# Optimization experiments

Measured on AMD Instinct MI355X. Metric: run time of the kernel, lower is better.

The kernel has to match this reference:

```python
import jax, jax.numpy as jnp
import numpy as np
import math

# irreps: (multiplicity, l). Parities omitted (they only label output irreps, not the math).
X_IRREPS = [(64, 0), (64, 1), (64, 2)]   # dim 64*(1+3+5) = 576
Y_IRREPS = [(1, 0), (1, 1), (1, 2)]      # dim 9 (spherical-harmonic-like features)
N = 32768


def _cg(j1, m1, j2, m2, j3, m3):
    """Condon-Shortley Clebsch-Gordan <j1 m1 j2 m2 | j3 m3> (Racah formula)."""
    if m1 + m2 != m3:
        return 0.0
    f = math.factorial
    pre = (2 * j3 + 1) * f(j3 + j1 - j2) * f(j3 - j1 + j2) * f(j1 + j2 - j3) / f(j1 + j2 + j3 + 1)
    pre *= f(j3 + m3) * f(j3 - m3) * f(j1 - m1) * f(j1 + m1) * f(j2 - m2) * f(j2 + m2)
    s = 0.0
    for k in range(0, j1 + j2 - j3 + 1):
        d = [j1 + j2 - j3 - k, j1 - m1 - k, j2 + m2 - k, j3 - j2 + m1 + k, j3 - j1 - m2 + k]
        if min(d) < 0:
            continue
        s += (-1) ** k / (f(k) * f(d[0]) * f(d[1]) * f(d[2]) * f(d[3]) * f(d[4]))
    return math.sqrt(pre) * s


def _w3j_complex(l1, l2, l3):
    """Wigner 3j in the complex spherical basis, index m+l."""
    C = np.zeros((2 * l1 + 1, 2 * l2 + 1, 2 * l3 + 1), dtype=np.complex128)
    for m1 in range(-l1, l1 + 1):
        for m2 in range(-l2, l2 + 1):
            m3 = -(m1 + m2)
            if abs(m3) > l3:
                continue
            C[m1 + l1, m2 + l2, m3 + l3] = ((-1) ** (l1 - l2 - m3)) / math.sqrt(2 * l3 + 1) * _cg(l1, m1, l2, m2, l3, -m3)
    return C


def _Q(l):
    """Complex->real spherical harmonics change of basis (unitary)."""
    q = np.zeros((2 * l + 1, 2 * l + 1), dtype=np.complex128)
    q[l, l] = 1.0
    s2 = 1.0 / math.sqrt(2.0)
    for m in range(1, l + 1):
        q[l + m, l - m] = s2
        q[l + m, l + m] = ((-1) ** m) * s2
        q[l - m, l - m] = 1j * s2
        q[l - m, l + m] = -1j * ((-1) ** m) * s2
    return q


def _w3j_real(l1, l2, l3):
    """Real-basis Wigner 3j: invariant under real irreps; unit Frobenius norm 1/sqrt(2l3+1) preserved."""
    T = np.einsum('ia,jb,kc,abc->ijk', _Q(l1), _Q(l2), _Q(l3), _w3j_complex(l1, l2, l3))
    re, im = np.real(T), np.imag(T)
    W = re if np.abs(re).sum() >= np.abs(im).sum() else im
    return np.ascontiguousarray(W.astype(np.float32))


W3J = {}
for _mu, _l1 in X_IRREPS:
    for _mv, _l2 in Y_IRREPS:
        for _l3 in range(abs(_l1 - _l2), _l1 + _l2 + 1):
            if (_l1, _l2, _l3) not in W3J:
                W3J[(_l1, _l2, _l3)] = jnp.asarray(_w3j_real(_l1, _l2, _l3))


def _splits(irreps):
    out, off = [], 0
    for mul, l in irreps:
        d = mul * (2 * l + 1)
        out.append((mul, l, off, off + d))
        off += d
    return out


def setup_inputs() -> dict:
    key = jax.random.key(0)
    kx, ky = jax.random.split(key)
    x = jax.random.normal(kx, (N, 576), dtype=jnp.float32)
    y = jax.random.normal(ky, (N, 9), dtype=jnp.float32)
    return {"x": x, "y": y}


def reference(x, y):
    """Full e3nn-style tensor product with 'component' normalization (alpha = sqrt(2*l3+1)).
    Output chunks are concatenated in (l1, l2, l3) iteration order."""
    chunks = []
    for mu, l1, a1, b1 in _splits(X_IRREPS):
        xc = x[:, a1:b1].reshape(-1, mu, 2 * l1 + 1)
        for mv, l2, a2, b2 in _splits(Y_IRREPS):
            yc = y[:, a2:b2].reshape(-1, mv, 2 * l2 + 1)
            for l3 in range(abs(l1 - l2), l1 + l2 + 1):
                w = W3J[(l1, l2, l3)]
                alpha = np.float32(math.sqrt(2 * l3 + 1))
                z = jnp.einsum('nui,nvj,ijk->nuvk', xc, yc, w) * alpha
                chunks.append(z.reshape(z.shape[0], mu * mv * (2 * l3 + 1)))
    return jnp.concatenate(chunks, axis=-1)
```

## Files before the change

kernel.cpp:

```cpp
#include <hip/hip_runtime.h>


#define NP 19

constexpr int P_L1[NP]  = {0,0,0, 1,1,1,1,1,1,1, 2,2,2,2,2,2,2,2,2};
constexpr int P_L2[NP]  = {0,1,2, 0,1,1,1,2,2,2, 0,1,1,1,2,2,2,2,2};
constexpr int P_L3[NP]  = {0,1,2, 1,0,1,2,1,2,3, 2,1,2,3,0,1,2,3,4};
constexpr int P_WOFF[NP] = {0,1,10,35,44,53,80,125,170,245,350,375,420,495,600,625,700,825,1000};
constexpr int P_ZOFF[NP] = {0,64,256,576,768,832,1024,1344,1536,1856,2304,2624,2816,3136,3584,3648,3840,4160,4608};
constexpr int WTOT = 1225;
constexpr int XD = 576, YD = 9, ZD = 5184;


__device__ inline double dfact(int n){ double r=1.0; for(int i=2;i<=n;++i) r*=(double)i; return r; }

__device__ double cgc(int j1,int m1,int j2,int m2,int j3,int m3){
  if (m1+m2 != m3) return 0.0;
  double pre = (double)(2*j3+1) * dfact(j3+j1-j2)*dfact(j3-j1+j2)*dfact(j1+j2-j3)/dfact(j1+j2+j3+1);
  pre *= dfact(j3+m3)*dfact(j3-m3)*dfact(j1-m1)*dfact(j1+m1)*dfact(j2-m2)*dfact(j2+m2);
  double s = 0.0;
  for (int k=0;k<=j1+j2-j3;++k){
    int d0=j1+j2-j3-k, d1=j1-m1-k, d2=j2+m2-k, d3=j3-j2+m1+k, d4=j3-j1-m2+k;
    if (d0<0||d1<0||d2<0||d3<0||d4<0) continue;
    double t = 1.0/(dfact(k)*dfact(d0)*dfact(d1)*dfact(d2)*dfact(d3)*dfact(d4));
    s += (k&1) ? -t : t;
  }
  return sqrt(pre)*s;
}

__device__ inline void Qv(int l,int r,int c,double& re,double& im){
  re=0.0; im=0.0;
  const double s2 = 0.70710678118654752440;
  if (r==l){ if (c==l) re=1.0; return; }
  if (r>l){ int m=r-l;
    if (c==l-m)      re = s2;
    else if (c==l+m) re = (m&1)? -s2 : s2;
  } else { int m=l-r;
    if (c==l-m)      im = s2;
    else if (c==l+m) im = (m&1)? s2 : -s2;
  }
}

__global__ void w3j_init(float* __restrict__ w){
  const int p = blockIdx.x;
  const int l1=P_L1[p], l2=P_L2[p], l3=P_L3[p];
  const int d1=2*l1+1, d2=2*l2+1, d3=2*l3+1;
  __shared__ double Cre[25];
  __shared__ double Tre[225];
  __shared__ double Tim[225];
  __shared__ int pick;
  const int t = threadIdx.x;

  if (t < d1*d2){
    int a=t/d2, b=t%d2;
    int m1=a-l1, m2=b-l2, m3=-(m1+m2);
    int am3 = m3<0 ? -m3 : m3;
    double v = 0.0;
    if (am3 <= l3){
      v = cgc(l1,m1,l2,m2,l3,-m3) / sqrt((double)(2*l3+1));
      if ((l1-l2-m3)&1) v = -v;
    }
    Cre[t] = v;
  }
  __syncthreads();

  const int ne = d1*d2*d3;
  for (int e=t; e<ne; e+=blockDim.x){
    int i = e/(d2*d3); int r = e%(d2*d3); int j = r/d3; int k = r%d3;
    double tre=0.0, tim=0.0;
    for (int a=0;a<d1;a++){
      for (int b=0;b<d2;b++){
        double cr = Cre[a*d2+b];
        if (cr == 0.0) continue;
        int m3 = -((a-l1)+(b-l2));
        int c = m3 + l3;
        if (c < 0 || c >= d3) continue;
        double q1r,q1i,q2r,q2i,q3r,q3i;
        Qv(l1,i,a,q1r,q1i);
        Qv(l2,j,b,q2r,q2i);
        Qv(l3,k,c,q3r,q3i);
        double pr = q1r*q2r - q1i*q2i;
        double pi = q1r*q2i + q1i*q2r;
        double rr = pr*q3r - pi*q3i;
        double ri = pr*q3i + pi*q3r;
        tre += rr*cr; tim += ri*cr;
      }
    }
    Tre[e]=tre; Tim[e]=tim;
  }
  __syncthreads();

  if (t==0){
    double sre=0.0, sim=0.0;
    for (int e=0;e<ne;e++){ sre += fabs(Tre[e]); sim += fabs(Tim[e]); }
    pick = (sre >= sim) ? 0 : 1;
  }
  __syncthreads();

  const double alpha = sqrt((double)(2*l3+1));
  for (int e=t; e<ne; e+=blockDim.x){
    double v = pick ? Tim[e] : Tre[e];
    w[P_WOFF[p]+e] = (float)(v*alpha);
  }
}


__global__ __launch_bounds__(256) void tp_main(const float* __restrict__ x,
                                               const float* __restrict__ y,
                                               const float* __restrict__ w,
                                               float* __restrict__ out,
                                               int nrow){
  __shared__ float ws[WTOT];
  for (int t=threadIdx.x; t<WTOT; t+=256) ws[t] = w[t];
  __syncthreads();

  const int u = threadIdx.x & 63;
  int row = blockIdx.x*4 + (threadIdx.x>>6);
  row = __builtin_amdgcn_readfirstlane(row);
  if (row >= nrow) return;

  const float* xr = x + (size_t)row*XD;
  const float* yr = y + (size_t)row*YD;
  float*       zr = out + (size_t)row*ZD;

  float yv[9];
  #pragma unroll
  for (int j=0;j<9;++j) yv[j] = yr[j];

  float xv0 = xr[u];
  float xv1[3];
  #pragma unroll
  for (int i=0;i<3;++i) xv1[i] = xr[64 + 3*u + i];
  float xv2[5];
  #pragma unroll
  for (int i=0;i<5;++i) xv2[i] = xr[256 + 5*u + i];

  #pragma unroll
  for (int p=0;p<NP;++p){
    const int l1=P_L1[p], l2=P_L2[p], l3=P_L3[p];
    const int d1=2*l1+1, d2=2*l2+1, d3=2*l3+1;
    const int yo = (l2==0) ? 0 : (l2==1 ? 1 : 4);

    float acc[9];
    #pragma unroll
    for (int k=0;k<d3;++k) acc[k] = 0.f;

    #pragma unroll
    for (int i=0;i<d1;++i){
      const float xi = (l1==0) ? xv0 : (l1==1 ? xv1[i] : xv2[i]);
      #pragma unroll
      for (int j=0;j<d2;++j){
        const float xy = xi * yv[yo+j];
        #pragma unroll
        for (int k=0;k<d3;++k)
          acc[k] += xy * ws[P_WOFF[p] + (i*d2+j)*d3 + k];
      }
    }

    float* zp = zr + P_ZOFF[p] + u*d3;
    #pragma unroll
    for (int k=0;k<d3;++k) zp[k] = acc[k];
  }
}


extern "C" void kernel_launch(void* const* d_in, const int* in_sizes, int n_in,
                              void* d_out, int out_size, void* d_ws, size_t ws_size,
                              hipStream_t stream) {
  const float* x = (const float*)d_in[0];
  const float* y = (const float*)d_in[1];
  float* out = (float*)d_out;
  float* w   = (float*)d_ws;
  const int nrow = in_sizes[0] / XD;

  hipLaunchKernelGGL(w3j_init, dim3(NP), dim3(256), 0, stream, w);
  const int nb = (nrow + 3) / 4;
  hipLaunchKernelGGL(tp_main, dim3(nb), dim3(256), 0, stream, x, y, w, out, nrow);
}
```

Before: 742.1 us.

## Compute Wigner 3j tables at compile time and skip zero-coefficient FMAs

```diff
diff --git a/kernel.cpp b/kernel.cpp
--- a/kernel.cpp
+++ b/kernel.cpp
@@ -6,15 +6,25 @@
 constexpr int P_L1[NP]  = {0,0,0, 1,1,1,1,1,1,1, 2,2,2,2,2,2,2,2,2};
 constexpr int P_L2[NP]  = {0,1,2, 0,1,1,1,2,2,2, 0,1,1,1,2,2,2,2,2};
 constexpr int P_L3[NP]  = {0,1,2, 1,0,1,2,1,2,3, 2,1,2,3,0,1,2,3,4};
-constexpr int P_WOFF[NP] = {0,1,10,35,44,53,80,125,170,245,350,375,420,495,600,625,700,825,1000};
 constexpr int P_ZOFF[NP] = {0,64,256,576,768,832,1024,1344,1536,1856,2304,2624,2816,3136,3584,3648,3840,4160,4608};
-constexpr int WTOT = 1225;
 constexpr int XD = 576, YD = 9, ZD = 5184;
 
 
-__device__ inline double dfact(int n){ double r=1.0; for(int i=2;i<=n;++i) r*=(double)i; return r; }
+constexpr double dfact(int n){ double r=1.0; for(int i=2;i<=n;++i) r*=(double)i; return r; }
+constexpr double cabs_(double x){ return x<0.0 ? -x : x; }
 
-__device__ double cgc(int j1,int m1,int j2,int m2,int j3,int m3){
+constexpr double csqrt(double x){
+  if (x<=0.0) return 0.0;
+  double y = x>1.0 ? x : 1.0;
+  for (int i=0;i<50;++i){
+    double ny = 0.5*(y + x/y);
+    if (ny == y) break;
+    y = ny;
+  }
+  return y;
+}
+
+constexpr double cgc(int j1,int m1,int j2,int m2,int j3,int m3){
   if (m1+m2 != m3) return 0.0;
   double pre = (double)(2*j3+1) * dfact(j3+j1-j2)*dfact(j3-j1+j2)*dfact(j1+j2-j3)/dfact(j1+j2+j3+1);
   pre *= dfact(j3+m3)*dfact(j3-m3)*dfact(j1-m1)*dfact(j1+m1)*dfact(j2-m2)*dfact(j2+m2);
@@ -25,10 +35,10 @@
     double t = 1.0/(dfact(k)*dfact(d0)*dfact(d1)*dfact(d2)*dfact(d3)*dfact(d4));
     s += (k&1) ? -t : t;
   }
-  return sqrt(pre)*s;
+  return csqrt(pre)*s;
 }
 
-__device__ inline void Qv(int l,int r,int c,double& re,double& im){
+constexpr void Qv(int l,int r,int c,double& re,double& im){
   re=0.0; im=0.0;
   const double s2 = 0.70710678118654752440;
   if (r==l){ if (c==l) re=1.0; return; }
@@ -41,79 +51,92 @@
   }
 }
 
-__global__ void w3j_init(float* __restrict__ w){
-  const int p = blockIdx.x;
-  const int l1=P_L1[p], l2=P_L2[p], l3=P_L3[p];
+struct PathTab { float v[225]; };
+
+constexpr PathTab make_path(int l1,int l2,int l3){
+  PathTab t{};
   const int d1=2*l1+1, d2=2*l2+1, d3=2*l3+1;
-  __shared__ double Cre[25];
-  __shared__ double Tre[225];
-  __shared__ double Tim[225];
-  __shared__ int pick;
-  const int t = threadIdx.x;
-
-  if (t < d1*d2){
-    int a=t/d2, b=t%d2;
+  double Cre[25]={};
+  for (int a=0;a<d1;++a) for (int b=0;b<d2;++b){
     int m1=a-l1, m2=b-l2, m3=-(m1+m2);
     int am3 = m3<0 ? -m3 : m3;
     double v = 0.0;
     if (am3 <= l3){
-      v = cgc(l1,m1,l2,m2,l3,-m3) / sqrt((double)(2*l3+1));
+      v = cgc(l1,m1,l2,m2,l3,-m3) / csqrt((double)(2*l3+1));
       if ((l1-l2-m3)&1) v = -v;
     }
-    Cre[t] = v;
+    Cre[a*d2+b] = v;
   }
-  __syncthreads();
-
-  const int ne = d1*d2*d3;
-  for (int e=t; e<ne; e+=blockDim.x){
+  double Tre[225]={}, Tim[225]={};
+  for (int e=0;e<d1*d2*d3;++e){
     int i = e/(d2*d3); int r = e%(d2*d3); int j = r/d3; int k = r%d3;
     double tre=0.0, tim=0.0;
-    for (int a=0;a<d1;a++){
-      for (int b=0;b<d2;b++){
-        double cr = Cre[a*d2+b];
-        if (cr == 0.0) continue;
-        int m3 = -((a-l1)+(b-l2));
-        int c = m3 + l3;
-        if (c < 0 || c >= d3) continue;
-        double q1r,q1i,q2r,q2i,q3r,q3i;
-        Qv(l1,i,a,q1r,q1i);
-        Qv(l2,j,b,q2r,q2i);
-        Qv(l3,k,c,q3r,q3i);
-        double pr = q1r*q2r - q1i*q2i;
-        double pi = q1r*q2i + q1i*q2r;
-        double rr = pr*q3r - pi*q3i;
-        double ri = pr*q3i + pi*q3r;
-        tre += rr*cr; tim += ri*cr;
-      }
+    for (int a=0;a<d1;++a) for (int b=0;b<d2;++b){
+      double cr = Cre[a*d2+b];
+      if (cr == 0.0) continue;
+      int m3 = -((a-l1)+(b-l2));
+      int c = m3 + l3;
+      if (c < 0 || c >= d3) continue;
+      double q1r=0,q1i=0,q2r=0,q2i=0,q3r=0,q3i=0;
+      Qv(l1,i,a,q1r,q1i);
+      Qv(l2,j,b,q2r,q2i);
+      Qv(l3,k,c,q3r,q3i);
+      double pr = q1r*q2r - q1i*q2i;
+      double pi = q1r*q2i + q1i*q2r;
+      tre += (pr*q3r - pi*q3i)*cr;
+      tim += (pr*q3i + pi*q3r)*cr;
     }
     Tre[e]=tre; Tim[e]=tim;
   }
-  __syncthreads();
-
-  if (t==0){
-    double sre=0.0, sim=0.0;
-    for (int e=0;e<ne;e++){ sre += fabs(Tre[e]); sim += fabs(Tim[e]); }
-    pick = (sre >= sim) ? 0 : 1;
+  double sre=0.0, sim=0.0;
+  for (int e=0;e<d1*d2*d3;++e){ sre += cabs_(Tre[e]); sim += cabs_(Tim[e]); }
+  const bool useim = (sim > sre);
+  const double alpha = csqrt((double)(2*l3+1));
+  for (int e=0;e<d1*d2*d3;++e){
+    double v = useim ? Tim[e] : Tre[e];
+    t.v[e] = (float)(v*alpha);
   }
-  __syncthreads();
-
-  const double alpha = sqrt((double)(2*l3+1));
-  for (int e=t; e<ne; e+=blockDim.x){
-    double v = pick ? Tim[e] : Tre[e];
-    w[P_WOFF[p]+e] = (float)(v*alpha);
-  }
+  return t;
 }
 
+template<int P> struct PathW { static constexpr PathTab t = make_path(P_L1[P],P_L2[P],P_L3[P]); };
+
+
+template<int P>
+__device__ __forceinline__ void do_path(float xv0, const float (&xv1)[3], const float (&xv2)[5],
+                                        const float (&yv)[9], float* __restrict__ zr, int u){
+  constexpr int l1=P_L1[P], l2=P_L2[P], l3=P_L3[P];
+  constexpr int d1=2*l1+1, d2=2*l2+1, d3=2*l3+1;
+  constexpr int yo = (l2==0) ? 0 : (l2==1 ? 1 : 4);
+
+  float acc[d3];
+  #pragma unroll
+  for (int k=0;k<d3;++k) acc[k] = 0.f;
+
+  #pragma unroll
+  for (int i=0;i<d1;++i){
+    const float xi = (l1==0) ? xv0 : (l1==1 ? xv1[i] : xv2[i]);
+    #pragma unroll
+    for (int j=0;j<d2;++j){
+      const float xy = xi * yv[yo+j];
+      #pragma unroll
+      for (int k=0;k<d3;++k){
+        const float wv = PathW<P>::t.v[(i*d2+j)*d3 + k];
+        if (wv != 0.0f)
+          acc[k] = __builtin_fmaf(xy, wv, acc[k]);
+      }
+    }
+  }
+
+  float* zp = zr + P_ZOFF[P] + u*d3;
+  #pragma unroll
+  for (int k=0;k<d3;++k) zp[k] = acc[k];
+}
 
 __global__ __launch_bounds__(256) void tp_main(const float* __restrict__ x,
                                                const float* __restrict__ y,
-                                               const float* __restrict__ w,
                                                float* __restrict__ out,
                                                int nrow){
-  __shared__ float ws[WTOT];
-  for (int t=threadIdx.x; t<WTOT; t+=256) ws[t] = w[t];
-  __syncthreads();
-
   const int u = threadIdx.x & 63;
   int row = blockIdx.x*4 + (threadIdx.x>>6);
   row = __builtin_amdgcn_readfirstlane(row);
@@ -135,32 +158,25 @@
   #pragma unroll
   for (int i=0;i<5;++i) xv2[i] = xr[256 + 5*u + i];
 
-  #pragma unroll
-  for (int p=0;p<NP;++p){
-    const int l1=P_L1[p], l2=P_L2[p], l3=P_L3[p];
-    const int d1=2*l1+1, d2=2*l2+1, d3=2*l3+1;
-    const int yo = (l2==0) ? 0 : (l2==1 ? 1 : 4);
-
-    float acc[9];
-    #pragma unroll
-    for (int k=0;k<d3;++k) acc[k] = 0.f;
-
-    #pragma unroll
-    for (int i=0;i<d1;++i){
-      const float xi = (l1==0) ? xv0 : (l1==1 ? xv1[i] : xv2[i]);
-      #pragma unroll
-      for (int j=0;j<d2;++j){
-        const float xy = xi * yv[yo+j];
-        #pragma unroll
-        for (int k=0;k<d3;++k)
-          acc[k] += xy * ws[P_WOFF[p] + (i*d2+j)*d3 + k];
-      }
-    }
-
-    float* zp = zr + P_ZOFF[p] + u*d3;
-    #pragma unroll
-    for (int k=0;k<d3;++k) zp[k] = acc[k];
-  }
+  do_path< 0>(xv0,xv1,xv2,yv,zr,u);
+  do_path< 1>(xv0,xv1,xv2,yv,zr,u);
+  do_path< 2>(xv0,xv1,xv2,yv,zr,u);
+  do_path< 3>(xv0,xv1,xv2,yv,zr,u);
+  do_path< 4>(xv0,xv1,xv2,yv,zr,u);
+  do_path< 5>(xv0,xv1,xv2,yv,zr,u);
+  do_path< 6>(xv0,xv1,xv2,yv,zr,u);
+  do_path< 7>(xv0,xv1,xv2,yv,zr,u);
+  do_path< 8>(xv0,xv1,xv2,yv,zr,u);
+  do_path< 9>(xv0,xv1,xv2,yv,zr,u);
+  do_path<10>(xv0,xv1,xv2,yv,zr,u);
+  do_path<11>(xv0,xv1,xv2,yv,zr,u);
+  do_path<12>(xv0,xv1,xv2,yv,zr,u);
+  do_path<13>(xv0,xv1,xv2,yv,zr,u);
+  do_path<14>(xv0,xv1,xv2,yv,zr,u);
+  do_path<15>(xv0,xv1,xv2,yv,zr,u);
+  do_path<16>(xv0,xv1,xv2,yv,zr,u);
+  do_path<17>(xv0,xv1,xv2,yv,zr,u);
+  do_path<18>(xv0,xv1,xv2,yv,zr,u);
 }
 
 
@@ -170,10 +186,7 @@
   const float* x = (const float*)d_in[0];
   const float* y = (const float*)d_in[1];
   float* out = (float*)d_out;
-  float* w   = (float*)d_ws;
   const int nrow = in_sizes[0] / XD;
-
-  hipLaunchKernelGGL(w3j_init, dim3(NP), dim3(256), 0, stream, w);
   const int nb = (nrow + 3) / 4;
-  hipLaunchKernelGGL(tp_main, dim3(nb), dim3(256), 0, stream, x, y, w, out, nrow);
+  hipLaunchKernelGGL(tp_main, dim3(nb), dim3(256), 0, stream, x, y, out, nrow);
 }
```

Result: slower. 757.2 us (+2.0%).
